# Kernel optimization log

Hardware: AMD Instinct MI355X
Metric: run time of the kernel (lower is better)

## Reference

```python
import jax, jax.numpy as jnp
import numpy as np

B, S, D = 128, 1024, 256
K = 512  # num_clusters


def setup_inputs() -> dict:
    key = jax.random.key(0)
    k1, = jax.random.split(key, 1)
    inputs = jax.random.normal(k1, (B, S, D), dtype=jnp.float32)
    # init centroids as the first K data points so no cluster is empty
    centroids = inputs.reshape(-1, D)[:K]
    return {"inputs": inputs, "centroids": centroids}


def reference(inputs, centroids):
    d = inputs.shape[-1]
    k = centroids.shape[0]
    x = inputs.reshape(-1, d)                      # [N, D]
    # squared euclidean distances via GEMM decomposition (avoids N x K x D tensor)
    x2 = jnp.sum(x * x, axis=1, keepdims=True)     # [N, 1]
    c2 = jnp.sum(centroids * centroids, axis=1)    # [K]
    dist = x2 - 2.0 * (x @ centroids.T) + c2       # [N, K]
    idx = jnp.argmin(dist, axis=-1)                # [N]
    clusters = jax.nn.one_hot(idx, k, dtype=x.dtype)   # [N, K]
    counts = jnp.sum(clusters, axis=0)             # [K]
    sums = jnp.einsum('nk,nd->kd', clusters, x)    # [K, D] scatter-reduce as GEMM
    new_centroids = sums / counts[:, None]         # [K, D]
    updated_centroids = 0.9 * centroids + 0.1 * new_centroids  # EMA update
    clusters_out = clusters.reshape(inputs.shape[:-1] + (k,))  # [B, S, K]
    return clusters_out, updated_centroids
```

## Files before the change

### kernel.cpp

```cpp
#include <hip/hip_runtime.h>
#include <hip/hip_fp16.h>

#define NPTS 131072
#define DIM  256
#define KTOT 512
#define GAP_T 0.0625f

typedef unsigned short u16;
typedef _Float16 half8 __attribute__((ext_vector_type(8)));
typedef float floatx4 __attribute__((ext_vector_type(4)));

#define WS_MAIN_NEED 8394816u

__global__ __launch_bounds__(64)
void c2_kernel(const float* __restrict__ c, double* __restrict__ c2) {
  int k = blockIdx.x;
  int lane = threadIdx.x;
  const float* row = c + (size_t)k * DIM;
  double s = 0.0;
#pragma unroll
  for (int r = 0; r < DIM / 64; ++r) {
    float v = row[r * 64 + lane];
    s += (double)v * (double)v;
  }
#pragma unroll
  for (int off = 32; off > 0; off >>= 1) s += __shfl_down(s, off);
  if (lane == 0) c2[k] = s;
}

__global__ __launch_bounds__(256)
void csplit_kernel(const float* __restrict__ c, u16* __restrict__ Ch, u16* __restrict__ Cl) {
  int id = blockIdx.x * 256 + threadIdx.x;
  int n = id >> 5;
  int cg = id & 31;
  int kc = cg >> 3, cc = cg & 7;
  const float* src = c + (size_t)n * DIM + cg * 8;
  half8 hv, lv;
#pragma unroll
  for (int e = 0; e < 8; ++e) {
    float f = src[e];
    _Float16 h = (_Float16)f;
    hv[e] = h;
    lv[e] = (_Float16)(f - (float)h);
  }
  size_t dst = (size_t)n * DIM + kc * 64 + (size_t)(cc ^ (n & 7)) * 8;
  *(half8*)(Ch + dst) = hv;
  *(half8*)(Cl + dst) = lv;
}

__device__ __forceinline__ void load_lds16(const void* g, void* l) {
  __builtin_amdgcn_global_load_lds((const __attribute__((address_space(1))) void*)g,
                                   (__attribute__((address_space(3))) void*)l, 16, 0, 0);
}

__global__ __launch_bounds__(256)
void gemm_topk_kernel(const float* __restrict__ x, const u16* __restrict__ Ch,
                      const u16* __restrict__ Cl, const double* __restrict__ c2,
                      float* __restrict__ pv1, int* __restrict__ pk1, float* __restrict__ pv2) {
  __shared__ __align__(16) unsigned char smem[128 * 132 * 4];
  __shared__ float rb_v[128], rb_v2[128];
  __shared__ int rb_k[128];
  u16* Ah = (u16*)smem;
  u16* Al = Ah + 8192;
  u16* Bh = Al + 8192;
  u16* Bl = Bh + 8192;

  const int tid = threadIdx.x;
  const int bx = blockIdx.x;
  const int nblk = bx & 3, mblk = bx >> 2;
  const int m0 = mblk * 128, n0 = nblk * 128;
  const int w = tid >> 6, lane = tid & 63;
  const int wm = (w & 1) * 64, wn = (w >> 1) * 64;
  const int lm = lane & 15, quad = lane >> 4;

  floatx4 acc[4][4] = {};

  for (int kc = 0; kc < 4; ++kc) {
    const int k0 = kc * 64;
    __syncthreads();
#pragma unroll
    for (int i = 0; i < 4; ++i) {
      int s = i * 256 + tid;
      int row = s >> 3, pos = s & 7;
      size_t go = (size_t)(n0 + row) * DIM + k0 + pos * 8;
      load_lds16(Ch + go, Bh + (size_t)s * 8);
      load_lds16(Cl + go, Bl + (size_t)s * 8);
    }
#pragma unroll
    for (int i = 0; i < 4; ++i) {
      int s = i * 256 + tid;
      int row = s >> 3, kg = s & 7;
      const float4* gx = (const float4*)(x + (size_t)(m0 + row) * DIM + k0 + kg * 8);
      float4 f0 = gx[0], f1 = gx[1];
      float fv[8] = {f0.x, f0.y, f0.z, f0.w, f1.x, f1.y, f1.z, f1.w};
      half8 hv, lv;
#pragma unroll
      for (int e = 0; e < 8; ++e) {
        _Float16 h = (_Float16)fv[e];
        hv[e] = h;
        lv[e] = (_Float16)(fv[e] - (float)h);
      }
      int pos = kg ^ (row & 7);
      *(half8*)(Ah + (size_t)row * 64 + pos * 8) = hv;
      *(half8*)(Al + (size_t)row * 64 + pos * 8) = lv;
    }
    __syncthreads();

#pragma unroll
    for (int s = 0; s < 2; ++s) {
      half8 ah[4], al[4], bh[4], bl[4];
#pragma unroll
      for (int t = 0; t < 4; ++t) {
        int m = wm + t * 16 + lm;
        int pa = ((s * 4 + quad) ^ (m & 7)) * 8;
        ah[t] = *(const half8*)(Ah + (size_t)m * 64 + pa);
        al[t] = *(const half8*)(Al + (size_t)m * 64 + pa);
        int n = wn + t * 16 + lm;
        int pb = ((s * 4 + quad) ^ (n & 7)) * 8;
        bh[t] = *(const half8*)(Bh + (size_t)n * 64 + pb);
        bl[t] = *(const half8*)(Bl + (size_t)n * 64 + pb);
      }
#pragma unroll
      for (int mt = 0; mt < 4; ++mt)
#pragma unroll
        for (int nt = 0; nt < 4; ++nt) {
          acc[mt][nt] = __builtin_amdgcn_mfma_f32_16x16x32_f16(ah[mt], bh[nt], acc[mt][nt], 0, 0, 0);
          acc[mt][nt] = __builtin_amdgcn_mfma_f32_16x16x32_f16(ah[mt], bl[nt], acc[mt][nt], 0, 0, 0);
          acc[mt][nt] = __builtin_amdgcn_mfma_f32_16x16x32_f16(al[mt], bh[nt], acc[mt][nt], 0, 0, 0);
        }
    }
  }

  __syncthreads();
  float* sc = (float*)smem;
  float c2f[4];
#pragma unroll
  for (int nt = 0; nt < 4; ++nt) c2f[nt] = (float)c2[n0 + wn + nt * 16 + lm];
#pragma unroll
  for (int mt = 0; mt < 4; ++mt)
#pragma unroll
    for (int nt = 0; nt < 4; ++nt)
#pragma unroll
      for (int r = 0; r < 4; ++r) {
        int m = wm + mt * 16 + quad * 4 + r;
        int n = wn + nt * 16 + lm;
        sc[m * 132 + n] = c2f[nt] - 2.0f * acc[mt][nt][r];
      }
  __syncthreads();

  {
    int r = tid >> 1, h = tid & 1;
    const float* rowp = sc + r * 132 + h * 64;
    float bv = 1e30f, sv = 1e30f;
    int bk = 0;
#pragma unroll 8
    for (int j = 0; j < 64; ++j) {
      float v = rowp[j];
      if (v < bv) { sv = bv; bv = v; bk = n0 + h * 64 + j; }
      else if (v < sv) sv = v;
    }
    if (h == 1) { rb_v[r] = bv; rb_k[r] = bk; rb_v2[r] = sv; }
    __syncthreads();
    if (h == 0) {
      float ov = rb_v[r], ov2 = rb_v2[r];
      int ok = rb_k[r];
      float fbv, fsv; int fbk;
      if (ov < bv) { fbv = ov; fbk = ok; fsv = fminf(bv, ov2); }
      else         { fbv = bv; fbk = bk; fsv = fminf(sv, ov); }
      int m = m0 + r;
      pv1[(size_t)nblk * NPTS + m] = fbv;
      pk1[(size_t)nblk * NPTS + m] = fbk;
      pv2[(size_t)nblk * NPTS + m] = fsv;
    }
  }
}

__global__ __launch_bounds__(256)
void combine_kernel(const float* __restrict__ pv1, const int* __restrict__ pk1,
                    const float* __restrict__ pv2, int* __restrict__ idx,
                    int* __restrict__ flagcnt, int* __restrict__ flaglist) {
  int m = blockIdx.x * 256 + threadIdx.x;
  float bv = 1e30f, sv = 1e30f;
  int bk = 0;
#pragma unroll
  for (int b = 0; b < 4; ++b) {
    float v1 = pv1[(size_t)b * NPTS + m];
    int k1 = pk1[(size_t)b * NPTS + m];
    float v2 = pv2[(size_t)b * NPTS + m];
    if (v1 < bv) { sv = fminf(bv, v2); bv = v1; bk = k1; }
    else { sv = fminf(sv, v1); }
  }
  idx[m] = bk;
  if (sv - bv < GAP_T) {
    int p = atomicAdd(flagcnt, 1);
    flaglist[p] = m;
  }
}

__global__ __launch_bounds__(256)
void refine_kernel(const float* __restrict__ x, const float* __restrict__ c,
                   const double* __restrict__ c2, const int* __restrict__ flagcnt,
                   const int* __restrict__ flaglist, int* __restrict__ idx) {
  __shared__ __align__(16) float xs[DIM];
  __shared__ double rv[256];
  __shared__ int rk[256];
  int cnt = *(volatile const int*)flagcnt;
  for (int i = blockIdx.x; i < cnt; i += gridDim.x) {
    __syncthreads();
    int m = flaglist[i];
    if (threadIdx.x < 64)
      ((float4*)xs)[threadIdx.x] = ((const float4*)(x + (size_t)m * DIM))[threadIdx.x];
    __syncthreads();
    double bestv = 1e300; int bestk = 0;
#pragma unroll
    for (int half = 0; half < 2; ++half) {
      int k = half * 256 + threadIdx.x;
      const float* crow = c + (size_t)k * DIM;
      double dacc = 0.0;
#pragma unroll
      for (int dc = 0; dc < 8; ++dc) {
        float f = 0.0f;
#pragma unroll
        for (int d = 0; d < 32; ++d) f = fmaf(xs[dc * 32 + d], crow[dc * 32 + d], f);
        dacc += (double)f;
      }
      double s = c2[k] - 2.0 * dacc;
      if (s < bestv || (s == bestv && k < bestk)) { bestv = s; bestk = k; }
    }
    rv[threadIdx.x] = bestv; rk[threadIdx.x] = bestk;
    __syncthreads();
    for (int off = 128; off > 0; off >>= 1) {
      if (threadIdx.x < off) {
        double v = rv[threadIdx.x + off]; int kk = rk[threadIdx.x + off];
        if (v < rv[threadIdx.x] || (v == rv[threadIdx.x] && kk < rk[threadIdx.x])) {
          rv[threadIdx.x] = v; rk[threadIdx.x] = kk;
        }
      }
      __syncthreads();
    }
    if (threadIdx.x == 0) idx[m] = rk[0];
  }
}

__global__ __launch_bounds__(256)
void onehot_kernel(const int* __restrict__ idx, float* __restrict__ out) {
  __shared__ int bk[32];
  int b = blockIdx.x;
  if (threadIdx.x < 32) bk[threadIdx.x] = idx[b * 32 + threadIdx.x];
  __syncthreads();
  float4* o = (float4*)(out + (size_t)b * 32 * KTOT);
#pragma unroll
  for (int j = 0; j < 16; ++j) {
    int f4 = j * 256 + threadIdx.x;
    int p = f4 >> 7;
    int n4 = (f4 & 127) * 4;
    int k = bk[p];
    float4 v;
    v.x = (k == n4 + 0) ? 1.0f : 0.0f;
    v.y = (k == n4 + 1) ? 1.0f : 0.0f;
    v.z = (k == n4 + 2) ? 1.0f : 0.0f;
    v.w = (k == n4 + 3) ? 1.0f : 0.0f;
    o[f4] = v;
  }
}

#define GB 4
#define SLICES 8
__global__ __launch_bounds__(256)
void sums_kernel(const float* __restrict__ x, const int* __restrict__ idx,
                 float* __restrict__ sums, int* __restrict__ counts) {
  const int groups = KTOT / GB;
  const int group = blockIdx.x % groups;
  const int slice = blockIdx.x / groups;
  const int kg0 = group * GB;
  const int tid = threadIdx.x;
  const int lane = tid & 63;
  const int w = tid >> 6;
  const int per_slice = NPTS / SLICES;
  const int nbeg = slice * per_slice;

  float4 acc[GB];
  int cnt[GB];
#pragma unroll
  for (int j = 0; j < GB; ++j) { acc[j] = make_float4(0.f, 0.f, 0.f, 0.f); cnt[j] = 0; }

  for (int it = 0; it < per_slice; it += 256) {
    int n = nbeg + it + tid;
    int k = idx[n];
#pragma unroll
    for (int j = 0; j < GB; ++j) {
      unsigned long long m = __ballot(k == kg0 + j);
      while (m) {
        int src = __ffsll((unsigned long long)m) - 1;
        int nn = __shfl(n, src);
        float4 v = ((const float4*)(x + (size_t)nn * DIM))[lane];
        acc[j].x += v.x; acc[j].y += v.y; acc[j].z += v.z; acc[j].w += v.w;
        cnt[j]++;
        m &= (m - 1);
      }
    }
  }

  __shared__ __align__(16) float lacc[4][GB][DIM];
  __shared__ int lcnt[4][GB];
#pragma unroll
  for (int j = 0; j < GB; ++j) ((float4*)&lacc[w][j][0])[lane] = acc[j];
  if (lane == 0) {
#pragma unroll
    for (int j = 0; j < GB; ++j) lcnt[w][j] = cnt[j];
  }
  __syncthreads();
#pragma unroll
  for (int j = 0; j < GB; ++j) {
    float s = lacc[0][j][tid] + lacc[1][j][tid] + lacc[2][j][tid] + lacc[3][j][tid];
    atomicAdd(&sums[(size_t)(kg0 + j) * DIM + tid], s);
  }
  if (tid < GB) {
    int ct = lcnt[0][tid] + lcnt[1][tid] + lcnt[2][tid] + lcnt[3][tid];
    atomicAdd(&counts[kg0 + tid], ct);
  }
}

__global__ __launch_bounds__(256)
void ema_kernel(const float* __restrict__ c, const float* __restrict__ sums,
                const int* __restrict__ counts, float* __restrict__ outc) {
  int k = blockIdx.x;
  int d = threadIdx.x;
  float cnt = (float)counts[k];
  size_t o = (size_t)k * DIM + d;
  float nc = sums[o] / cnt;
  outc[o] = 0.9f * c[o] + 0.1f * nc;
}

#define MP 64
#define KT 64
#define DT 32
__global__ __launch_bounds__(256, 2)
void assign_kernel_r1(const float* __restrict__ x, const float* __restrict__ c,
                      const double* __restrict__ c2, float* __restrict__ out,
                      int* __restrict__ idx_out) {
  __shared__ __align__(16) float xs[DIM * MP];
  __shared__ __align__(16) float cs[DT * KT];
  const int tid = threadIdx.x;
  const int p0 = blockIdx.x * MP;
  const int tp = tid & 15;
  const int tk = tid >> 4;
  {
    const int p = tid >> 2;
    const int dg = tid & 3;
    const float4* x4 = (const float4*)(x + (size_t)(p0 + p) * DIM);
#pragma unroll
    for (int r = 0; r < 16; ++r) {
      int d4 = r * 4 + dg;
      float4 v = x4[d4];
      int dbase = d4 * 4;
      xs[(dbase + 0) * MP + p] = v.x;
      xs[(dbase + 1) * MP + p] = v.y;
      xs[(dbase + 2) * MP + p] = v.z;
      xs[(dbase + 3) * MP + p] = v.w;
    }
  }
  double best[4]; int bestk[4];
#pragma unroll
  for (int i = 0; i < 4; ++i) { best[i] = 1e300; bestk[i] = 0; }
  for (int kc = 0; kc < KTOT / KT; ++kc) {
    const int k0 = kc * KT;
    double dacc[4][4];
#pragma unroll
    for (int i = 0; i < 4; ++i)
#pragma unroll
      for (int j = 0; j < 4; ++j) dacc[i][j] = 0.0;
    for (int dc = 0; dc < DIM / DT; ++dc) {
      __syncthreads();
      {
        const int kl = tid >> 2;
        const int dg = tid & 3;
        const float4* c4 = (const float4*)(c + (size_t)(k0 + kl) * DIM + dc * DT);
#pragma unroll
        for (int h = 0; h < 2; ++h) {
          int dq = h * 4 + dg;
          float4 v = c4[dq];
          int dbase = dq * 4;
          cs[(dbase + 0) * KT + kl] = v.x;
          cs[(dbase + 1) * KT + kl] = v.y;
          cs[(dbase + 2) * KT + kl] = v.z;
          cs[(dbase + 3) * KT + kl] = v.w;
        }
      }
      __syncthreads();
      float acc[4][4];
#pragma unroll
      for (int i = 0; i < 4; ++i)
#pragma unroll
        for (int j = 0; j < 4; ++j) acc[i][j] = 0.0f;
#pragma unroll
      for (int d = 0; d < DT; ++d) {
        float4 xv = ((const float4*)(xs + (size_t)(dc * DT + d) * MP))[tp];
        float4 cv = ((const float4*)(cs + (size_t)d * KT))[tk];
        float xa[4] = {xv.x, xv.y, xv.z, xv.w};
        float ca[4] = {cv.x, cv.y, cv.z, cv.w};
#pragma unroll
        for (int i = 0; i < 4; ++i)
#pragma unroll
          for (int j = 0; j < 4; ++j) acc[i][j] = fmaf(xa[i], ca[j], acc[i][j]);
      }
#pragma unroll
      for (int i = 0; i < 4; ++i)
#pragma unroll
        for (int j = 0; j < 4; ++j) dacc[i][j] += (double)acc[i][j];
    }
#pragma unroll
    for (int j = 0; j < 4; ++j) {
      int k = k0 + tk * 4 + j;
      double c2v = c2[k];
#pragma unroll
      for (int i = 0; i < 4; ++i) {
        double s = c2v - 2.0 * dacc[i][j];
        if (s < best[i]) { best[i] = s; bestk[i] = k; }
      }
    }
  }
  __syncthreads();
  double* redv = (double*)cs;
  int* redk = (int*)xs;
  int* bk = (int*)xs + 1024;
#pragma unroll
  for (int i = 0; i < 4; ++i) {
    int p = tp * 4 + i;
    redv[tk * MP + p] = best[i];
    redk[tk * MP + p] = bestk[i];
  }
  __syncthreads();
  if (tid < MP) {
    int p = tid;
    double bv = redv[p]; int bkk = redk[p];
#pragma unroll
    for (int t = 1; t < 16; ++t) {
      double v = redv[t * MP + p]; int kk = redk[t * MP + p];
      if (v < bv || (v == bv && kk < bkk)) { bv = v; bkk = kk; }
    }
    bk[p] = bkk;
    idx_out[p0 + p] = bkk;
  }
  __syncthreads();
  float* orow = out + (size_t)p0 * KTOT;
  for (int l = tid; l < MP * KTOT; l += 256) {
    int p = l >> 9;
    int k = l & (KTOT - 1);
    orow[l] = (k == bk[p]) ? 1.0f : 0.0f;
  }
}

extern "C" void kernel_launch(void* const* d_in, const int* in_sizes, int n_in,
                              void* d_out, int out_size, void* d_ws, size_t ws_size,
                              hipStream_t stream) {
  const float* x = (const float*)d_in[0];
  const float* c = (const float*)d_in[1];
  float* out = (float*)d_out;
  float* outc = out + (size_t)NPTS * KTOT;

  char* ws = (char*)d_ws;

  if (ws_size >= WS_MAIN_NEED) {
    double* c2   = (double*)(ws + 0);
    u16* Ch      = (u16*)(ws + 4096);
    u16* Cl      = (u16*)(ws + 266240);
    int* idx     = (int*)(ws + 528384);
    float* pv1   = (float*)(ws + 1052672);
    int* pk1     = (int*)(ws + 3149824);
    float* pv2   = (float*)(ws + 5246976);
    float* sums  = (float*)(ws + 7344128);
    int* counts  = (int*)(ws + 7868416);
    int* flagcnt = (int*)(ws + 7870464);
    int* flaglist= (int*)(ws + 7870528);

    hipMemsetAsync(sums, 0, (size_t)(KTOT * DIM + KTOT) * 4, stream);
    hipMemsetAsync(flagcnt, 0, 64, stream);
    c2_kernel<<<KTOT, 64, 0, stream>>>(c, c2);
    csplit_kernel<<<64, 256, 0, stream>>>(c, Ch, Cl);
    gemm_topk_kernel<<<4096, 256, 0, stream>>>(x, Ch, Cl, c2, pv1, pk1, pv2);
    combine_kernel<<<NPTS / 256, 256, 0, stream>>>(pv1, pk1, pv2, idx, flagcnt, flaglist);
    refine_kernel<<<256, 256, 0, stream>>>(x, c, c2, flagcnt, flaglist, idx);
    onehot_kernel<<<NPTS / 32, 256, 0, stream>>>(idx, out);
    sums_kernel<<<(KTOT / GB) * SLICES, 256, 0, stream>>>(x, idx, sums, counts);
    ema_kernel<<<KTOT, DIM, 0, stream>>>(c, sums, counts, outc);
  } else {
    double* c2  = (double*)ws;
    int* idx    = (int*)(ws + 4096);
    float* sums = (float*)(ws + 4096 + 524288);
    int* counts = (int*)(ws + 4096 + 524288 + 524288);
    hipMemsetAsync(sums, 0, (size_t)(KTOT * DIM + KTOT) * 4, stream);
    c2_kernel<<<KTOT, 64, 0, stream>>>(c, c2);
    assign_kernel_r1<<<NPTS / MP, 256, 0, stream>>>(x, c, c2, out, idx);
    sums_kernel<<<(KTOT / GB) * SLICES, 256, 0, stream>>>(x, idx, sums, counts);
    ema_kernel<<<KTOT, DIM, 0, stream>>>(c, sums, counts, outc);
  }
}
```

Measured before the change: 735.6 us.

## Replace per-cluster scan sums with histogram, prefix-scan, scatter and gather-sum

```diff
diff --git a/kernel.cpp b/kernel.cpp
--- a/kernel.cpp
+++ b/kernel.cpp
@@ -264,6 +264,92 @@
   }
 }
 
+__global__ __launch_bounds__(256)
+void hist_kernel(const int* __restrict__ idx, int* __restrict__ counts) {
+  __shared__ int h[KTOT];
+  int t = threadIdx.x;
+#pragma unroll
+  for (int i = 0; i < KTOT / 256; ++i) h[i * 256 + t] = 0;
+  __syncthreads();
+  int base = blockIdx.x * 1024 + t;
+#pragma unroll
+  for (int j = 0; j < 4; ++j) atomicAdd(&h[idx[base + j * 256]], 1);
+  __syncthreads();
+#pragma unroll
+  for (int i = 0; i < KTOT / 256; ++i) {
+    int v = h[i * 256 + t];
+    if (v) atomicAdd(&counts[i * 256 + t], v);
+  }
+}
+
+__global__ __launch_bounds__(512)
+void scan_kernel(const int* __restrict__ counts, int* __restrict__ offsets,
+                 int* __restrict__ cursors) {
+  __shared__ int s[KTOT];
+  int t = threadIdx.x;
+  int mine = counts[t];
+  s[t] = mine;
+  __syncthreads();
+  for (int off = 1; off < KTOT; off <<= 1) {
+    int v = (t >= off) ? s[t - off] : 0;
+    __syncthreads();
+    s[t] += v;
+    __syncthreads();
+  }
+  int excl = s[t] - mine;
+  offsets[t] = excl;
+  cursors[t] = excl;
+  if (t == KTOT - 1) offsets[KTOT] = s[t];
+}
+
+__global__ __launch_bounds__(256)
+void scatter_kernel(const int* __restrict__ idx, int* __restrict__ cursors,
+                    int* __restrict__ plist) {
+  int base = blockIdx.x * 1024 + threadIdx.x;
+#pragma unroll
+  for (int j = 0; j < 4; ++j) {
+    int n = base + j * 256;
+    int k = idx[n];
+    int pos = atomicAdd(&cursors[k], 1);
+    plist[pos] = n;
+  }
+}
+
+__global__ __launch_bounds__(256)
+void gathersum_kernel(const float* __restrict__ x, const int* __restrict__ plist,
+                      const int* __restrict__ offsets, float* __restrict__ sums) {
+  int k = blockIdx.x >> 2, slice = blockIdx.x & 3;
+  int beg = offsets[k], end = offsets[k + 1];
+  int cnt = end - beg;
+  int s0 = beg + ((cnt * slice) >> 2);
+  int s1 = beg + ((cnt * (slice + 1)) >> 2);
+  if (s1 <= s0) return;
+  int w = threadIdx.x >> 6, lane = threadIdx.x & 63;
+  float4 acc = make_float4(0.f, 0.f, 0.f, 0.f);
+  for (int i = s0 + w; i < s1; i += 4) {
+    int pid = plist[i];
+    float4 v = ((const float4*)x)[(size_t)pid * 64 + lane];
+    acc.x += v.x; acc.y += v.y; acc.z += v.z; acc.w += v.w;
+  }
+  __shared__ __align__(16) float lacc[4][DIM];
+  ((float4*)&lacc[w][0])[lane] = acc;
+  __syncthreads();
+  int t = threadIdx.x;
+  float v = lacc[0][t] + lacc[1][t] + lacc[2][t] + lacc[3][t];
+  atomicAdd(&sums[(size_t)k * DIM + t], v);
+}
+
+__global__ __launch_bounds__(256)
+void ema_kernel(const float* __restrict__ c, const float* __restrict__ sums,
+                const int* __restrict__ counts, float* __restrict__ outc) {
+  int k = blockIdx.x;
+  int d = threadIdx.x;
+  float cnt = (float)counts[k];
+  size_t o = (size_t)k * DIM + d;
+  float nc = sums[o] / cnt;
+  outc[o] = 0.9f * c[o] + 0.1f * nc;
+}
+
 #define GB 4
 #define SLICES 8
 __global__ __launch_bounds__(256)
@@ -319,17 +405,6 @@
     int ct = lcnt[0][tid] + lcnt[1][tid] + lcnt[2][tid] + lcnt[3][tid];
     atomicAdd(&counts[kg0 + tid], ct);
   }
-}
-
-__global__ __launch_bounds__(256)
-void ema_kernel(const float* __restrict__ c, const float* __restrict__ sums,
-                const int* __restrict__ counts, float* __restrict__ outc) {
-  int k = blockIdx.x;
-  int d = threadIdx.x;
-  float cnt = (float)counts[k];
-  size_t o = (size_t)k * DIM + d;
-  float nc = sums[o] / cnt;
-  outc[o] = 0.9f * c[o] + 0.1f * nc;
 }
 
 #define MP 64
@@ -473,6 +548,9 @@
     int* counts  = (int*)(ws + 7868416);
     int* flagcnt = (int*)(ws + 7870464);
     int* flaglist= (int*)(ws + 7870528);
+    int* offsets = (int*)(ws + 1052672);
+    int* cursors = (int*)(ws + 1052672 + 4096);
+    int* plist   = (int*)(ws + 5246976);
 
     hipMemsetAsync(sums, 0, (size_t)(KTOT * DIM + KTOT) * 4, stream);
     hipMemsetAsync(flagcnt, 0, 64, stream);
@@ -482,7 +560,10 @@
     combine_kernel<<<NPTS / 256, 256, 0, stream>>>(pv1, pk1, pv2, idx, flagcnt, flaglist);
     refine_kernel<<<256, 256, 0, stream>>>(x, c, c2, flagcnt, flaglist, idx);
     onehot_kernel<<<NPTS / 32, 256, 0, stream>>>(idx, out);
-    sums_kernel<<<(KTOT / GB) * SLICES, 256, 0, stream>>>(x, idx, sums, counts);
+    hist_kernel<<<NPTS / 1024, 256, 0, stream>>>(idx, counts);
+    scan_kernel<<<1, 512, 0, stream>>>(counts, offsets, cursors);
+    scatter_kernel<<<NPTS / 1024, 256, 0, stream>>>(idx, cursors, plist);
+    gathersum_kernel<<<KTOT * 4, 256, 0, stream>>>(x, plist, offsets, sums);
     ema_kernel<<<KTOT, DIM, 0, stream>>>(c, sums, counts, outc);
   } else {
     double* c2  = (double*)ws;
```

Result: slower. 1.110 ms (+50.8%).
